# Performance work log

Hardware: AMD Instinct MI355X
Metric: run time of the kernel (lower is better)

Reference implementation:

```python
import jax, jax.numpy as jnp
import numpy as np

GAMMA = 20.0
NUM_VIEWS = 64

def setup_inputs() -> dict:
    key = jax.random.key(0)
    k1, k2, k3 = jax.random.split(key, 3)
    B, L, D = 16, 4096, 1024
    v_pad = jax.random.normal(k1, (B, L, D), dtype=jnp.float32)
    v_len = jax.random.randint(k2, (B,), 1, L + 1, dtype=jnp.int32)
    # (T, H, W) per sample; only W/H ratio matters -> square 64x64 grid
    grid_thws = jnp.tile(jnp.array([[1, 64, 64]], dtype=jnp.int32), (B, 1))
    centers = jax.random.uniform(k3, (B, NUM_VIEWS, 2), dtype=jnp.float32)
    return {"v_pad": v_pad, "v_len": v_len, "grid_thws": grid_thws, "centers": centers}

def reference(v_pad, v_len, grid_thws, centers):
    B, L, D = v_pad.shape
    Lv = v_len.astype(jnp.float32)                      # [B]
    H = grid_thws[:, 1].astype(jnp.float32)
    W = grid_thws[:, 2].astype(jnp.float32)
    # adaptive 2D mapping of the 1D token sequence
    W_eff = jnp.maximum(1, jnp.round(jnp.sqrt(Lv * (W / H))).astype(jnp.int32))  # [B]
    H_eff = jnp.maximum(1, jnp.ceil(Lv / W_eff.astype(jnp.float32)).astype(jnp.int32))
    idx = jnp.arange(L, dtype=jnp.int32)                # [L]
    We = W_eff[:, None]
    He = H_eff[:, None]
    x = (idx[None, :] % We).astype(jnp.float32) / We.astype(jnp.float32)   # [B, L]
    y = (idx[None, :] // We).astype(jnp.float32) / He.astype(jnp.float32)  # [B, L]
    coords = jnp.stack([x, y], axis=-1)                 # [B, L, 2]
    # squared distance from each view center to each token coord
    diff = centers[:, :, None, :] - coords[:, None, :, :]   # [B, V, L, 2]
    dist_sq = jnp.sum(diff * diff, axis=-1)                 # [B, V, L]
    valid = (idx[None, :] < v_len[:, None]).astype(v_pad.dtype)  # [B, L]
    m = jnp.exp(-GAMMA * dist_sq) * valid[:, None, :]       # [B, V, L]
    numerator = jnp.einsum('bvl,bld->bvd', m, v_pad)        # [B, V, D]
    denominator = jnp.sum(m, axis=-1, keepdims=True) + 1e-6 # [B, V, 1]
    return numerator / denominator
```

## Files before the change

### kernel.cpp

```cpp
#include <hip/hip_runtime.h>
#include <math.h>
#include <stdint.h>


constexpr int VV      = 64;
constexpr int DC      = 256;
constexpr int KS      = 64;
constexpr int NTH     = 256;
constexpr int ST      = 270;
constexpr int SXY_MAX = 512;

typedef __attribute__((ext_vector_type(8))) short short8;
typedef __attribute__((ext_vector_type(4))) float f32x4;

static __device__ __forceinline__ unsigned short f2bf(float f) {
    unsigned u = __builtin_bit_cast(unsigned, f);
    u += 0x7fffu + ((u >> 16) & 1u);
    return (unsigned short)(u >> 16);
}

__global__ __launch_bounds__(NTH)
void dvs_mfma(const float* __restrict__ v_pad, const int* __restrict__ v_len,
              const int* __restrict__ grid_thws, const float* __restrict__ centers,
              float* __restrict__ num_part,
              float* __restrict__ den_part,
              int B, int L, int D, int K)
{
    const int kblk = blockIdx.x, dcb = blockIdx.y, b = blockIdx.z;
    const int tid  = threadIdx.x;
    const int d0   = dcb * DC;
    const int lane = tid & 63;
    const int wave = tid >> 6;

    __shared__ __align__(16) unsigned short smA[512 * 8];
    __shared__ __align__(16) unsigned short smB[KS][ST];
    __shared__ float2 sxy[SXY_MAX];
    __shared__ float  sden[4][VV];

    const int   Lv = v_len[b];
    const float Hf = (float)grid_thws[b*3 + 1];
    const float Wf = (float)grid_thws[b*3 + 2];
    const float sq = sqrtf((float)Lv * (Wf / Hf));
    int W_eff = (int)rintf(sq);                       if (W_eff < 1) W_eff = 1;
    int H_eff = (int)ceilf((float)Lv / (float)W_eff); if (H_eff < 1) H_eff = 1;
    const float invW = 1.f / (float)W_eff, invH = 1.f / (float)H_eff;

    const int chunk = (Lv + K - 1) / K;
    const int l0 = kblk * chunk;
    const int l1 = min(l0 + chunk, Lv);

    const int    av  = tid & 63;
    const int    aq  = tid >> 6;
    const float2 ctr = ((const float2*)centers)[(size_t)b * VV + av];
    const int    amf = av >> 4, ar = av & 15;
    float denacc = 0.f;

    const int d4 = tid & 63;
    const int lq = tid >> 6;

    const int fcol = lane & 15, foct = lane >> 4;

    f32x4 acc[4][4];
#pragma unroll
    for (int i = 0; i < 4; ++i)
#pragma unroll
        for (int j = 0; j < 4; ++j) acc[i][j] = f32x4{0.f, 0.f, 0.f, 0.f};

    const float* vp_b = v_pad + (size_t)b * L * D + d0;

    for (int st = l0; st < l1; st += SXY_MAX) {
        const int st1 = min(st + SXY_MAX, l1);
        __syncthreads();
        for (int i = tid; i < st1 - st; i += NTH) {
            const int l   = st + i;
            const int row = l / W_eff;
            const int col = l - row * W_eff;
            sxy[i] = make_float2((float)col * invW, (float)row * invH);
        }
        __syncthreads();

        for (int lt = st; lt < st1; lt += KS) {
            float4 ld[16];
#pragma unroll
            for (int it = 0; it < 16; ++it) {
                const int l = lt + it * 4 + lq;
                ld[it] = make_float4(0.f, 0.f, 0.f, 0.f);
                if (l < st1)
                    ld[it] = *(const float4*)(vp_b + (size_t)l * D + d4 * 4);
            }
            __syncthreads();

#pragma unroll
            for (int it = 0; it < 16; ++it) {
                const int lrow = it * 4 + lq;
                unsigned* w = (unsigned*)&smB[lrow][d4 * 4];
                unsigned p0 = (unsigned)f2bf(ld[it].x) | ((unsigned)f2bf(ld[it].y) << 16);
                unsigned p1 = (unsigned)f2bf(ld[it].z) | ((unsigned)f2bf(ld[it].w) << 16);
                w[0] = p0;
                w[1] = p1;
            }

#pragma unroll
            for (int ks = 0; ks < 2; ++ks) {
                union { unsigned short h[8]; short8 s; } ap;
#pragma unroll
                for (int j = 0; j < 8; ++j) {
                    const int kl = ks * 32 + aq * 8 + j;
                    const int l  = lt + kl;
                    float m = 0.f;
                    if (l < st1) {
                        const float2 xy = sxy[(lt - st) + kl];
                        const float dx = ctr.x - xy.x, dy = ctr.y - xy.y;
                        m = __expf(-20.f * (dx * dx + dy * dy));
                    }
                    denacc += m;
                    ap.h[j] = f2bf(m);
                }
                ((short8*)smA)[(ks * 4 + amf) * 64 + aq * 16 + ar] = ap.s;
            }
            __syncthreads();

#pragma unroll
            for (int ks = 0; ks < 2; ++ks) {
                short8 af[4];
#pragma unroll
                for (int mf = 0; mf < 4; ++mf)
                    af[mf] = ((const short8*)smA)[(ks * 4 + mf) * 64 + lane];

#pragma unroll
                for (int nf = 0; nf < 4; ++nf) {
                    const int colx  = wave * 64 + nf * 16 + fcol;
                    const int kbase = ks * 32 + foct * 8;
                    union { unsigned short h[8]; short8 s; } bf;
#pragma unroll
                    for (int j = 0; j < 8; ++j)
                        bf.h[j] = smB[kbase + j][colx];
#pragma unroll
                    for (int mf = 0; mf < 4; ++mf)
                        acc[mf][nf] = __builtin_amdgcn_mfma_f32_16x16x32_bf16(
                            af[mf], bf.s, acc[mf][nf], 0, 0, 0);
                }
            }
        }
    }

    sden[aq][av] = denacc;
    __syncthreads();
    if (dcb == 0 && tid < VV) {
        den_part[((size_t)b * K + kblk) * VV + tid] =
            sden[0][tid] + sden[1][tid] + sden[2][tid] + sden[3][tid];
    }

    float* basep = num_part + ((size_t)b * K + kblk) * VV * (size_t)D + d0 + wave * 64;
#pragma unroll
    for (int mf = 0; mf < 4; ++mf) {
#pragma unroll
        for (int nf = 0; nf < 4; ++nf) {
            const int colx = nf * 16 + fcol;
            const int row0 = mf * 16 + foct * 4;
#pragma unroll
            for (int r = 0; r < 4; ++r)
                basep[(size_t)(row0 + r) * D + colx] = acc[mf][nf][r];
        }
    }
}

__global__ __launch_bounds__(256)
void dvs_reduce(const float* __restrict__ num_part,
                const float* __restrict__ den_part,
                float*       __restrict__ out,
                int B, int D, int K, int total)
{
    const int idx = blockIdx.x * 256 + threadIdx.x;
    if (idx >= total) return;
    const int d  = idx % D;
    const int bv = idx / D;
    const int b  = bv / VV;
    const int v  = bv - b * VV;

    float den = 1e-6f;
    float num = 0.0f;
    for (int k = 0; k < K; ++k) {
        den += den_part[((size_t)b * K + k) * VV + v];
        num += num_part[(((size_t)b * K + k) * VV + v) * (size_t)D + d];
    }
    out[idx] = num / den;
}

extern "C" void kernel_launch(void* const* d_in, const int* in_sizes, int n_in,
                              void* d_out, int out_size, void* d_ws, size_t ws_size,
                              hipStream_t stream)
{
    const float* v_pad     = (const float*)d_in[0];
    const int*   v_len     = (const int*)d_in[1];
    const int*   grid_thws = (const int*)d_in[2];
    const float* centers   = (const float*)d_in[3];
    float*       out       = (float*)d_out;

    const int B = in_sizes[1];
    const int V = VV;
    const int D = out_size / (B * V);
    const int L = in_sizes[0] / (B * D);

    int K = 8;
    const size_t per_k = ((size_t)B * V * D + (size_t)B * V) * sizeof(float);
    while (K > 1 && (size_t)K * per_k > ws_size) K >>= 1;

    float* num_part = (float*)d_ws;
    float* den_part = num_part + (size_t)B * K * V * D;

    dim3 grid1(K, D / DC, B);
    dvs_mfma<<<grid1, NTH, 0, stream>>>(v_pad, v_len, grid_thws, centers,
                                        num_part, den_part, B, L, D, K);

    const int total = B * V * D;
    dvs_reduce<<<(total + 255) / 256, 256, 0, stream>>>(num_part, den_part, out,
                                                        B, D, K, total);
}
```

Measured before the change: 52.59 us.

## Halve D-chunk per block, prefetch next v_pad tile into registers, vectorize reduce

The D chunk per block is cut from 256 to 128 columns, which doubles the grid and halves the accumulator tiles per wave. The global loads of the next 64-row v_pad tile are now issued before the MFMA phase of the current tile, so memory latency overlaps with compute. An extra barrier is added per tile to protect the shared buffer. The reduce kernel now processes float4 vectors and multiplies by the reciprocal of the denominator. Costs include more blocks recomputing the Gaussian weights and one more sync per tile.

```diff
diff --git a/kernel.cpp b/kernel.cpp
--- a/kernel.cpp
+++ b/kernel.cpp
@@ -4,10 +4,10 @@
 
 
 constexpr int VV      = 64;
-constexpr int DC      = 256;
+constexpr int DC      = 128;
 constexpr int KS      = 64;
 constexpr int NTH     = 256;
-constexpr int ST      = 270;
+constexpr int ST      = 134;
 constexpr int SXY_MAX = 512;
 
 typedef __attribute__((ext_vector_type(8))) short short8;
@@ -55,22 +55,32 @@
     const int    amf = av >> 4, ar = av & 15;
     float denacc = 0.f;
 
-    const int d4 = tid & 63;
-    const int lq = tid >> 6;
+    const int sd   = tid & 31;
+    const int srow = tid >> 5;
 
     const int fcol = lane & 15, foct = lane >> 4;
 
-    f32x4 acc[4][4];
-#pragma unroll
-    for (int i = 0; i < 4; ++i)
-#pragma unroll
-        for (int j = 0; j < 4; ++j) acc[i][j] = f32x4{0.f, 0.f, 0.f, 0.f};
+    f32x4 acc[4][2];
+#pragma unroll
+    for (int i = 0; i < 4; ++i) {
+        acc[i][0] = f32x4{0.f, 0.f, 0.f, 0.f};
+        acc[i][1] = f32x4{0.f, 0.f, 0.f, 0.f};
+    }
 
     const float* vp_b = v_pad + (size_t)b * L * D + d0;
 
     for (int st = l0; st < l1; st += SXY_MAX) {
         const int st1 = min(st + SXY_MAX, l1);
         __syncthreads();
+
+        float4 ld[8];
+#pragma unroll
+        for (int it = 0; it < 8; ++it) {
+            const int l = st + it * 8 + srow;
+            ld[it] = make_float4(0.f, 0.f, 0.f, 0.f);
+            if (l < st1)
+                ld[it] = *(const float4*)(vp_b + (size_t)l * D + sd * 4);
+        }
         for (int i = tid; i < st1 - st; i += NTH) {
             const int l   = st + i;
             const int row = l / W_eff;
@@ -80,26 +90,13 @@
         __syncthreads();
 
         for (int lt = st; lt < st1; lt += KS) {
-            float4 ld[16];
-#pragma unroll
-            for (int it = 0; it < 16; ++it) {
-                const int l = lt + it * 4 + lq;
-                ld[it] = make_float4(0.f, 0.f, 0.f, 0.f);
-                if (l < st1)
-                    ld[it] = *(const float4*)(vp_b + (size_t)l * D + d4 * 4);
-            }
-            __syncthreads();
-
-#pragma unroll
-            for (int it = 0; it < 16; ++it) {
-                const int lrow = it * 4 + lq;
-                unsigned* w = (unsigned*)&smB[lrow][d4 * 4];
-                unsigned p0 = (unsigned)f2bf(ld[it].x) | ((unsigned)f2bf(ld[it].y) << 16);
-                unsigned p1 = (unsigned)f2bf(ld[it].z) | ((unsigned)f2bf(ld[it].w) << 16);
-                w[0] = p0;
-                w[1] = p1;
-            }
-
+#pragma unroll
+            for (int it = 0; it < 8; ++it) {
+                const int lrow = it * 8 + srow;
+                unsigned* w = (unsigned*)&smB[lrow][sd * 4];
+                w[0] = (unsigned)f2bf(ld[it].x) | ((unsigned)f2bf(ld[it].y) << 16);
+                w[1] = (unsigned)f2bf(ld[it].z) | ((unsigned)f2bf(ld[it].w) << 16);
+            }
 #pragma unroll
             for (int ks = 0; ks < 2; ++ks) {
                 union { unsigned short h[8]; short8 s; } ap;
@@ -120,6 +117,17 @@
             }
             __syncthreads();
 
+            const int ltn = lt + KS;
+            if (ltn < st1) {
+#pragma unroll
+                for (int it = 0; it < 8; ++it) {
+                    const int l = ltn + it * 8 + srow;
+                    ld[it] = make_float4(0.f, 0.f, 0.f, 0.f);
+                    if (l < st1)
+                        ld[it] = *(const float4*)(vp_b + (size_t)l * D + sd * 4);
+                }
+            }
+
 #pragma unroll
             for (int ks = 0; ks < 2; ++ks) {
                 short8 af[4];
@@ -128,8 +136,8 @@
                     af[mf] = ((const short8*)smA)[(ks * 4 + mf) * 64 + lane];
 
 #pragma unroll
-                for (int nf = 0; nf < 4; ++nf) {
-                    const int colx  = wave * 64 + nf * 16 + fcol;
+                for (int nf = 0; nf < 2; ++nf) {
+                    const int colx  = wave * 32 + nf * 16 + fcol;
                     const int kbase = ks * 32 + foct * 8;
                     union { unsigned short h[8]; short8 s; } bf;
 #pragma unroll
@@ -141,6 +149,7 @@
                             af[mf], bf.s, acc[mf][nf], 0, 0, 0);
                 }
             }
+            __syncthreads();
         }
     }
 
@@ -151,11 +160,11 @@
             sden[0][tid] + sden[1][tid] + sden[2][tid] + sden[3][tid];
     }
 
-    float* basep = num_part + ((size_t)b * K + kblk) * VV * (size_t)D + d0 + wave * 64;
+    float* basep = num_part + ((size_t)b * K + kblk) * VV * (size_t)D + d0 + wave * 32;
 #pragma unroll
     for (int mf = 0; mf < 4; ++mf) {
 #pragma unroll
-        for (int nf = 0; nf < 4; ++nf) {
+        for (int nf = 0; nf < 2; ++nf) {
             const int colx = nf * 16 + fcol;
             const int row0 = mf * 16 + foct * 4;
 #pragma unroll
@@ -169,22 +178,27 @@
 void dvs_reduce(const float* __restrict__ num_part,
                 const float* __restrict__ den_part,
                 float*       __restrict__ out,
-                int B, int D, int K, int total)
+                int B, int D, int K, int total4)
 {
     const int idx = blockIdx.x * 256 + threadIdx.x;
-    if (idx >= total) return;
-    const int d  = idx % D;
-    const int bv = idx / D;
-    const int b  = bv / VV;
-    const int v  = bv - b * VV;
-
-    float den = 1e-6f;
-    float num = 0.0f;
+    if (idx >= total4) return;
+    const int dq4 = D / 4;
+    const int d4  = idx % dq4;
+    const int bv  = idx / dq4;
+    const int b   = bv / VV;
+    const int v   = bv - b * VV;
+
+    float  den = 1e-6f;
+    float4 num = make_float4(0.f, 0.f, 0.f, 0.f);
     for (int k = 0; k < K; ++k) {
         den += den_part[((size_t)b * K + k) * VV + v];
-        num += num_part[(((size_t)b * K + k) * VV + v) * (size_t)D + d];
-    }
-    out[idx] = num / den;
+        const float4 p = ((const float4*)(num_part +
+                          (((size_t)b * K + k) * VV + v) * (size_t)D))[d4];
+        num.x += p.x; num.y += p.y; num.z += p.z; num.w += p.w;
+    }
+    const float inv = 1.0f / den;
+    float4 o = make_float4(num.x * inv, num.y * inv, num.z * inv, num.w * inv);
+    ((float4*)out)[(size_t)bv * dq4 + d4] = o;
 }
 
 extern "C" void kernel_launch(void* const* d_in, const int* in_sizes, int n_in,
@@ -213,7 +227,7 @@
     dvs_mfma<<<grid1, NTH, 0, stream>>>(v_pad, v_len, grid_thws, centers,
                                         num_part, den_part, B, L, D, K);
 
-    const int total = B * V * D;
-    dvs_reduce<<<(total + 255) / 256, 256, 0, stream>>>(num_part, den_part, out,
-                                                        B, D, K, total);
-}
+    const int total4 = B * V * D / 4;
+    dvs_reduce<<<(total4 + 255) / 256, 256, 0, stream>>>(num_part, den_part, out,
+                                                         B, D, K, total4);
+}
```

Result: faster. 43.30 us (-17.7%).

## Fuse split-K reduce into single kernel with narrower D tiles and register prefetch

Applied to the files above, without the earlier changes.

Removes the split-K partition and the separate reduction kernel: each block now processes the whole valid sequence for a 64-wide slice of D using 8 waves, normalizing by the denominator in-kernel and writing the output directly. The next tile of v_pad is prefetched into registers while the MFMA work of the current tile runs. This eliminates the workspace write/read of partial numerators, at the cost of fewer, longer-running blocks, narrower per-row memory segments, and load imbalance across samples with different lengths.

```diff
diff --git a/kernel.cpp b/kernel.cpp
--- a/kernel.cpp
+++ b/kernel.cpp
@@ -4,10 +4,10 @@
 
 
 constexpr int VV      = 64;
-constexpr int DC      = 256;
+constexpr int DC      = 64;
 constexpr int KS      = 64;
-constexpr int NTH     = 256;
-constexpr int ST      = 270;
+constexpr int NTH     = 512;
+constexpr int ST2     = 66;
 constexpr int SXY_MAX = 512;
 
 typedef __attribute__((ext_vector_type(8))) short short8;
@@ -20,22 +20,21 @@
 }
 
 __global__ __launch_bounds__(NTH)
-void dvs_mfma(const float* __restrict__ v_pad, const int* __restrict__ v_len,
-              const int* __restrict__ grid_thws, const float* __restrict__ centers,
-              float* __restrict__ num_part,
-              float* __restrict__ den_part,
-              int B, int L, int D, int K)
+void dvs_fused(const float* __restrict__ v_pad, const int* __restrict__ v_len,
+               const int* __restrict__ grid_thws, const float* __restrict__ centers,
+               float* __restrict__ out, int B, int L, int D)
 {
-    const int kblk = blockIdx.x, dcb = blockIdx.y, b = blockIdx.z;
+    const int dcb = blockIdx.x, b = blockIdx.y;
     const int tid  = threadIdx.x;
     const int d0   = dcb * DC;
     const int lane = tid & 63;
     const int wave = tid >> 6;
 
-    __shared__ __align__(16) unsigned short smA[512 * 8];
-    __shared__ __align__(16) unsigned short smB[KS][ST];
+    __shared__ __align__(16) unsigned short smA[8 * 64 * 8];
+    __shared__ __align__(16) unsigned short smB[KS][ST2];
     __shared__ float2 sxy[SXY_MAX];
-    __shared__ float  sden[4][VV];
+    __shared__ float  sden[8][VV];
+    __shared__ float  sinv[VV];
 
     const int   Lv = v_len[b];
     const float Hf = (float)grid_thws[b*3 + 1];
@@ -45,32 +44,39 @@
     int H_eff = (int)ceilf((float)Lv / (float)W_eff); if (H_eff < 1) H_eff = 1;
     const float invW = 1.f / (float)W_eff, invH = 1.f / (float)H_eff;
 
-    const int chunk = (Lv + K - 1) / K;
-    const int l0 = kblk * chunk;
-    const int l1 = min(l0 + chunk, Lv);
+    const int l1 = Lv;
 
     const int    av  = tid & 63;
     const int    aq  = tid >> 6;
     const float2 ctr = ((const float2*)centers)[(size_t)b * VV + av];
     const int    amf = av >> 4, ar = av & 15;
+    const int    aks = aq >> 2, aoct = aq & 3;
     float denacc = 0.f;
 
-    const int d4 = tid & 63;
-    const int lq = tid >> 6;
+    const int brow = tid >> 4;
+    const int bc4  = tid & 15;
 
     const int fcol = lane & 15, foct = lane >> 4;
+    const int nf   = wave & 3;
+    const int mfb  = (wave >> 2) * 2;
 
-    f32x4 acc[4][4];
-#pragma unroll
-    for (int i = 0; i < 4; ++i)
-#pragma unroll
-        for (int j = 0; j < 4; ++j) acc[i][j] = f32x4{0.f, 0.f, 0.f, 0.f};
+    f32x4 acc[2];
+    acc[0] = f32x4{0.f, 0.f, 0.f, 0.f};
+    acc[1] = f32x4{0.f, 0.f, 0.f, 0.f};
 
     const float* vp_b = v_pad + (size_t)b * L * D + d0;
 
-    for (int st = l0; st < l1; st += SXY_MAX) {
+    float4 ld[2];
+#pragma unroll
+    for (int p = 0; p < 2; ++p) {
+        const int l = p * 32 + brow;
+        ld[p] = make_float4(0.f, 0.f, 0.f, 0.f);
+        if (l < l1)
+            ld[p] = *(const float4*)(vp_b + (size_t)l * D + bc4 * 4);
+    }
+
+    for (int st = 0; st < l1; st += SXY_MAX) {
         const int st1 = min(st + SXY_MAX, l1);
-        __syncthreads();
         for (int i = tid; i < st1 - st; i += NTH) {
             const int l   = st + i;
             const int row = l / W_eff;
@@ -80,35 +86,21 @@
         __syncthreads();
 
         for (int lt = st; lt < st1; lt += KS) {
-            float4 ld[16];
 #pragma unroll
-            for (int it = 0; it < 16; ++it) {
-                const int l = lt + it * 4 + lq;
-                ld[it] = make_float4(0.f, 0.f, 0.f, 0.f);
-                if (l < st1)
-                    ld[it] = *(const float4*)(vp_b + (size_t)l * D + d4 * 4);
+            for (int p = 0; p < 2; ++p) {
+                const int lrow = p * 32 + brow;
+                unsigned* w = (unsigned*)&smB[lrow][bc4 * 4];
+                w[0] = (unsigned)f2bf(ld[p].x) | ((unsigned)f2bf(ld[p].y) << 16);
+                w[1] = (unsigned)f2bf(ld[p].z) | ((unsigned)f2bf(ld[p].w) << 16);
             }
-            __syncthreads();
-
-#pragma unroll
-            for (int it = 0; it < 16; ++it) {
-                const int lrow = it * 4 + lq;
-                unsigned* w = (unsigned*)&smB[lrow][d4 * 4];
-                unsigned p0 = (unsigned)f2bf(ld[it].x) | ((unsigned)f2bf(ld[it].y) << 16);
-                unsigned p1 = (unsigned)f2bf(ld[it].z) | ((unsigned)f2bf(ld[it].w) << 16);
-                w[0] = p0;
-                w[1] = p1;
-            }
-
-#pragma unroll
-            for (int ks = 0; ks < 2; ++ks) {
+            {
                 union { unsigned short h[8]; short8 s; } ap;
 #pragma unroll
                 for (int j = 0; j < 8; ++j) {
-                    const int kl = ks * 32 + aq * 8 + j;
+                    const int kl = aq * 8 + j;
                     const int l  = lt + kl;
                     float m = 0.f;
-                    if (l < st1) {
+                    if (l < l1) {
                         const float2 xy = sxy[(lt - st) + kl];
                         const float dx = ctr.x - xy.x, dy = ctr.y - xy.y;
                         m = __expf(-20.f * (dx * dx + dy * dy));
@@ -116,75 +108,60 @@
                     denacc += m;
                     ap.h[j] = f2bf(m);
                 }
-                ((short8*)smA)[(ks * 4 + amf) * 64 + aq * 16 + ar] = ap.s;
+                ((short8*)smA)[(aks * 4 + amf) * 64 + aoct * 16 + ar] = ap.s;
             }
             __syncthreads();
 
+            const int ltn = lt + KS;
+            if (ltn < l1) {
+#pragma unroll
+                for (int p = 0; p < 2; ++p) {
+                    const int l = ltn + p * 32 + brow;
+                    ld[p] = make_float4(0.f, 0.f, 0.f, 0.f);
+                    if (l < l1)
+                        ld[p] = *(const float4*)(vp_b + (size_t)l * D + bc4 * 4);
+                }
+            }
+
 #pragma unroll
             for (int ks = 0; ks < 2; ++ks) {
-                short8 af[4];
+                short8 af[2];
 #pragma unroll
-                for (int mf = 0; mf < 4; ++mf)
-                    af[mf] = ((const short8*)smA)[(ks * 4 + mf) * 64 + lane];
+                for (int i = 0; i < 2; ++i)
+                    af[i] = ((const short8*)smA)[(ks * 4 + mfb + i) * 64 + lane];
 
+                const int kbase = ks * 32 + foct * 8;
+                union { unsigned short h[8]; short8 s; } bf;
 #pragma unroll
-                for (int nf = 0; nf < 4; ++nf) {
-                    const int colx  = wave * 64 + nf * 16 + fcol;
-                    const int kbase = ks * 32 + foct * 8;
-                    union { unsigned short h[8]; short8 s; } bf;
+                for (int j = 0; j < 8; ++j)
+                    bf.h[j] = smB[kbase + j][nf * 16 + fcol];
 #pragma unroll
-                    for (int j = 0; j < 8; ++j)
-                        bf.h[j] = smB[kbase + j][colx];
-#pragma unroll
-                    for (int mf = 0; mf < 4; ++mf)
-                        acc[mf][nf] = __builtin_amdgcn_mfma_f32_16x16x32_bf16(
-                            af[mf], bf.s, acc[mf][nf], 0, 0, 0);
-                }
+                for (int i = 0; i < 2; ++i)
+                    acc[i] = __builtin_amdgcn_mfma_f32_16x16x32_bf16(
+                        af[i], bf.s, acc[i], 0, 0, 0);
             }
+            __syncthreads();
         }
     }
 
     sden[aq][av] = denacc;
     __syncthreads();
-    if (dcb == 0 && tid < VV) {
-        den_part[((size_t)b * K + kblk) * VV + tid] =
-            sden[0][tid] + sden[1][tid] + sden[2][tid] + sden[3][tid];
+    if (tid < VV) {
+        float s = 1e-6f;
+#pragma unroll
+        for (int r = 0; r < 8; ++r) s += sden[r][tid];
+        sinv[tid] = 1.0f / s;
     }
+    __syncthreads();
 
-    float* basep = num_part + ((size_t)b * K + kblk) * VV * (size_t)D + d0 + wave * 64;
+    float* outp = out + (size_t)b * VV * D + d0 + nf * 16 + fcol;
 #pragma unroll
-    for (int mf = 0; mf < 4; ++mf) {
+    for (int i = 0; i < 2; ++i) {
+        const int row0 = (mfb + i) * 16 + foct * 4;
 #pragma unroll
-        for (int nf = 0; nf < 4; ++nf) {
-            const int colx = nf * 16 + fcol;
-            const int row0 = mf * 16 + foct * 4;
-#pragma unroll
-            for (int r = 0; r < 4; ++r)
-                basep[(size_t)(row0 + r) * D + colx] = acc[mf][nf][r];
-        }
+        for (int r = 0; r < 4; ++r)
+            outp[(size_t)(row0 + r) * D] = acc[i][r] * sinv[row0 + r];
     }
-}
-
-__global__ __launch_bounds__(256)
-void dvs_reduce(const float* __restrict__ num_part,
-                const float* __restrict__ den_part,
-                float*       __restrict__ out,
-                int B, int D, int K, int total)
-{
-    const int idx = blockIdx.x * 256 + threadIdx.x;
-    if (idx >= total) return;
-    const int d  = idx % D;
-    const int bv = idx / D;
-    const int b  = bv / VV;
-    const int v  = bv - b * VV;
-
-    float den = 1e-6f;
-    float num = 0.0f;
-    for (int k = 0; k < K; ++k) {
-        den += den_part[((size_t)b * K + k) * VV + v];
-        num += num_part[(((size_t)b * K + k) * VV + v) * (size_t)D + d];
-    }
-    out[idx] = num / den;
 }
 
 extern "C" void kernel_launch(void* const* d_in, const int* in_sizes, int n_in,
@@ -198,22 +175,10 @@
     float*       out       = (float*)d_out;
 
     const int B = in_sizes[1];
-    const int V = VV;
-    const int D = out_size / (B * V);
+    const int D = out_size / (B * VV);
     const int L = in_sizes[0] / (B * D);
 
-    int K = 8;
-    const size_t per_k = ((size_t)B * V * D + (size_t)B * V) * sizeof(float);
-    while (K > 1 && (size_t)K * per_k > ws_size) K >>= 1;
-
-    float* num_part = (float*)d_ws;
-    float* den_part = num_part + (size_t)B * K * V * D;
-
-    dim3 grid1(K, D / DC, B);
-    dvs_mfma<<<grid1, NTH, 0, stream>>>(v_pad, v_len, grid_thws, centers,
-                                        num_part, den_part, B, L, D, K);
-
-    const int total = B * V * D;
-    dvs_reduce<<<(total + 255) / 256, 256, 0, stream>>>(num_part, den_part, out,
-                                                        B, D, K, total);
+    dim3 grid(D / DC, B);
+    dvs_fused<<<grid, NTH, 0, stream>>>(v_pad, v_len, grid_thws, centers,
+                                        out, B, L, D);
 }
```

After: 80.53 us. +53.1%, slower.
